# Performance work log

Hardware: AMD Instinct MI355X
Metric: run time of the kernel (lower is better)

The kernel has to match this reference:

```python
import jax, jax.numpy as jnp
import numpy as np

N_QUBITS = 4
N_LAYERS = 2
BATCH = 524288


def _apply_1q(state, U, wire, batched):
    """Apply a 2x2 gate U on `wire`. state: [B,2,2,2,2]; U: [B,2,2] if batched else [2,2]."""
    ax = wire + 1
    s = jnp.moveaxis(state, ax, 1)
    if batched:
        s = jnp.einsum('bij,bj...->bi...', U, s)
    else:
        s = jnp.einsum('ij,bj...->bi...', U, s)
    return jnp.moveaxis(s, 1, ax)


def _apply_cnot(state, control, target):
    cax, tax = control + 1, target + 1
    s0 = jnp.take(state, 0, axis=cax)
    s1 = jnp.take(state, 1, axis=cax)
    t_ax = tax - 1 if tax > cax else tax  # target axis after removing control axis
    s1 = jnp.flip(s1, axis=t_ax)
    return jnp.stack([s0, s1], axis=cax)


def _circuit(x, weight):
    B = x.shape[0]
    # Angle encoding: RY(tanh(x_i) * pi) per wire (per-sample angles)
    theta = jnp.tanh(x) * jnp.pi  # [B, 4]
    state = jnp.zeros((B,) + (2,) * N_QUBITS, jnp.complex64)
    state = state.at[(slice(None),) + (0,) * N_QUBITS].set(1.0)
    for q in range(N_QUBITS):
        h = theta[:, q] * 0.5
        c, s = jnp.cos(h), jnp.sin(h)
        Ury = jnp.stack([jnp.stack([c, -s], -1), jnp.stack([s, c], -1)], -2).astype(jnp.complex64)  # [B,2,2]
        state = _apply_1q(state, Ury, q, batched=True)
    for layer in range(N_LAYERS):
        for q in range(N_QUBITS):
            hy = weight[layer, q, 0] * 0.5
            cy, sy = jnp.cos(hy), jnp.sin(hy)
            Uy = jnp.stack([jnp.stack([cy, -sy]), jnp.stack([sy, cy])]).astype(jnp.complex64)
            state = _apply_1q(state, Uy, q, batched=False)
            hz = weight[layer, q, 1] * 0.5
            ez = jnp.exp(-1j * hz.astype(jnp.complex64))
            z0 = jnp.zeros((), jnp.complex64)
            Uz = jnp.stack([jnp.stack([ez, z0]), jnp.stack([z0, jnp.conj(ez)])])
            state = _apply_1q(state, Uz, q, batched=False)
        for q in range(N_QUBITS):
            state = _apply_cnot(state, q, (q + 1) % N_QUBITS)
    # <Z_i> = P(bit_i = 0) - P(bit_i = 1)
    probs = jnp.abs(state) ** 2  # [B,2,2,2,2] float32
    outs = []
    for q in range(N_QUBITS):
        other_axes = tuple(a for a in range(1, N_QUBITS + 1) if a != q + 1)
        marg = probs.sum(other_axes)  # [B,2]
        outs.append(marg[:, 0] - marg[:, 1])
    return jnp.stack(outs, axis=-1).astype(jnp.float32)  # [B,4]


def setup_inputs() -> dict:
    key = jax.random.key(0)
    kx, kw = jax.random.split(key)
    x = jax.random.normal(kx, (BATCH, N_QUBITS), dtype=jnp.float32)
    weight = jax.random.normal(kw, (N_LAYERS, N_QUBITS, 2), dtype=jnp.float32) * 0.1
    return {"x": x, "weight": weight}


def reference(x, weight):
    return _circuit(x, weight)
```

## Files before the change

kernel.cpp:

```cpp
#include <hip/hip_runtime.h>
#include <math.h>


#define HALF_PI_F 1.57079632679489661923f

__global__ __launch_bounds__(256) void build_C4(
    const float* __restrict__ weight,
    float4* __restrict__ C4g)
{
    __shared__ float cw[16], sw[16];
    __shared__ float Ur[16][16], Ui[16][16];
    __shared__ float A[4][16][16];

    const int tid = threadIdx.x;
    if (tid < 16) {
        float h = 0.5f * weight[tid];
        __sincosf(h, &sw[tid], &cw[tid]);
    }
    __syncthreads();

    if (tid < 16) {
        const int col = tid;
        float re[16], im[16];
        #pragma unroll
        for (int i = 0; i < 16; ++i) { re[i] = 0.f; im[i] = 0.f; }
        re[col] = 1.f;

        #pragma unroll
        for (int layer = 0; layer < 2; ++layer) {
            #pragma unroll
            for (int q = 0; q < 4; ++q) {
                float cy = cw[layer*8 + q*2 + 0];
                float sy = sw[layer*8 + q*2 + 0];
                float cz = cw[layer*8 + q*2 + 1];
                float sz = sw[layer*8 + q*2 + 1];
                int st = 8 >> q;
                #pragma unroll
                for (int i = 0; i < 16; ++i) {
                    if (i & st) continue;
                    int j = i | st;
                    float r0 = re[i], r1 = re[j], i0 = im[i], i1 = im[j];
                    float nr0 = cy*r0 - sy*r1;
                    float nr1 = sy*r0 + cy*r1;
                    float ni0 = cy*i0 - sy*i1;
                    float ni1 = sy*i0 + cy*i1;
                    re[i] = nr0*cz + ni0*sz;
                    im[i] = ni0*cz - nr0*sz;
                    re[j] = nr1*cz - ni1*sz;
                    im[j] = ni1*cz + nr1*sz;
                }
            }
            #pragma unroll
            for (int q = 0; q < 4; ++q) {
                int cb = 8 >> q;
                int tb = 8 >> ((q + 1) & 3);
                #pragma unroll
                for (int i = 0; i < 16; ++i) {
                    if ((i & cb) && !(i & tb)) {
                        int j = i | tb;
                        float tr = re[i]; re[i] = re[j]; re[j] = tr;
                        float ti = im[i]; im[i] = im[j]; im[j] = ti;
                    }
                }
            }
        }
        #pragma unroll
        for (int i = 0; i < 16; ++i) { Ur[i][col] = re[i]; Ui[i][col] = im[i]; }
    }
    __syncthreads();

    for (int e = tid; e < 1024; e += 256) {
        int q = e >> 8, j = (e >> 4) & 15, k = e & 15;
        float sum = 0.f;
        for (int i = 0; i < 16; ++i) {
            float t = Ur[i][j]*Ur[i][k] + Ui[i][j]*Ui[i][k];
            sum += (i & (8 >> q)) ? -t : t;
        }
        A[q][j][k] = sum;
    }
    __syncthreads();

    if (tid < 100) {
        const int pu[10] = {0,0,0,0,1,1,1,2,2,3};
        const int pv[10] = {0,1,2,3,1,2,3,2,3,3};
        int pi = tid / 10, qi = tid % 10;
        int u = pu[pi], v = pv[pi], r = pu[qi], sI = pv[qi];
        int a1s[2] = {u, v}, a2s[2] = {v, u};
        int b1s[2] = {r, sI}, b2s[2] = {sI, r};
        int na = (u == v) ? 1 : 2;
        int nb = (r == sI) ? 1 : 2;
        float acc[4] = {0.f, 0.f, 0.f, 0.f};
        for (int ia = 0; ia < na; ++ia)
            for (int ib = 0; ib < nb; ++ib) {
                int j = a1s[ia]*4 + b1s[ib];
                int k = a2s[ia]*4 + b2s[ib];
                #pragma unroll
                for (int q = 0; q < 4; ++q) acc[q] += A[q][j][k];
            }
        C4g[tid] = float4{acc[0], acc[1], acc[2], acc[3]};
    }
}

__global__ __launch_bounds__(256) void qmain(
    const float* __restrict__ x,
    const float4* __restrict__ C4g,
    float* __restrict__ out,
    int B)
{
    const int s0 = blockIdx.x * 256 + threadIdx.x;

    float4 xv = (s0 < B) ? reinterpret_cast<const float4*>(x)[s0]
                         : float4{0.f, 0.f, 0.f, 0.f};

    const int pu[10] = {0,0,0,0,1,1,1,2,2,3};
    const int pv[10] = {0,1,2,3,1,2,3,2,3,3};

    float P[10], Q[10];
    {
        float xs[4] = {xv.x, xv.y, xv.z, xv.w};
        float c[4], s[4];
        #pragma unroll
        for (int q = 0; q < 4; ++q) {
            float e = __expf(2.f * xs[q]);
            float uu = __builtin_amdgcn_rcpf(e + 1.f);
            float rr = 0.5f * uu;
            c[q] = __builtin_amdgcn_sinf(rr);
            s[q] = __builtin_amdgcn_cosf(rr);
        }
        float a4[4] = {c[0]*c[1], c[0]*s[1], s[0]*c[1], s[0]*s[1]};
        float b4[4] = {c[2]*c[3], c[2]*s[3], s[2]*c[3], s[2]*s[3]};
        #pragma unroll
        for (int i2 = 0; i2 < 10; ++i2) {
            P[i2] = a4[pu[i2]] * a4[pv[i2]];
            Q[i2] = b4[pu[i2]] * b4[pv[i2]];
        }
    }

    float z0 = 0.f, z1 = 0.f, z2 = 0.f, z3 = 0.f;
    #pragma unroll
    for (int pi = 0; pi < 10; ++pi) {
        float t0 = 0.f, t1 = 0.f, t2 = 0.f, t3 = 0.f;
        #pragma unroll
        for (int qi = 0; qi < 10; ++qi) {
            float4 cv = C4g[pi*10 + qi];
            float qv = Q[qi];
            t0 = fmaf(cv.x, qv, t0);
            t1 = fmaf(cv.y, qv, t1);
            t2 = fmaf(cv.z, qv, t2);
            t3 = fmaf(cv.w, qv, t3);
        }
        float pvf = P[pi];
        z0 = fmaf(pvf, t0, z0);
        z1 = fmaf(pvf, t1, z1);
        z2 = fmaf(pvf, t2, z2);
        z3 = fmaf(pvf, t3, z3);
    }

    if (s0 < B)
        reinterpret_cast<float4*>(out)[s0] = float4{z0, z1, z2, z3};
}

extern "C" void kernel_launch(void* const* d_in, const int* in_sizes, int n_in,
                              void* d_out, int out_size, void* d_ws, size_t ws_size,
                              hipStream_t stream) {
    const float* x = (const float*)d_in[0];
    const float* w = (const float*)d_in[1];
    float* out = (float*)d_out;
    float4* C4g = (float4*)d_ws;
    int B = in_sizes[0] / 4;

    build_C4<<<1, 256, 0, stream>>>(w, C4g);
    int grid = (B + 255) / 256;
    qmain<<<grid, 256, 0, stream>>>(x, C4g, out, B);
}
```

Measured before the change: 70.79 us.

## Apply fixed circuit unitary via fp16 MFMA instead of quadratic-form coefficients

The precompute kernel now writes the 16x16 fixed unitary (real and imaginary parts) in fp16 MFMA fragment layout, replacing the 100-entry quadratic-form coefficient table. The main kernel builds each sample's 16-amplitude product state in shared memory and multiplies it by the unitary with two 16x16x16 fp16 MFMAs per 16 samples. It then forms probabilities and reduces the Z expectations with cross-lane shuffles. This swaps about 400 scalar FMAs per sample for matrix-core work, at the cost of fp16 precision loss on the state and unitary, plus a block barrier and LDS traffic.

```diff
diff --git a/kernel.cpp b/kernel.cpp
--- a/kernel.cpp
+++ b/kernel.cpp
@@ -2,15 +2,22 @@
 #include <math.h>
 
 
-#define HALF_PI_F 1.57079632679489661923f
+typedef _Float16 f16x4 __attribute__((ext_vector_type(4)));
+typedef _Float16 f16x8 __attribute__((ext_vector_type(8)));
+typedef float f32x4 __attribute__((ext_vector_type(4)));
 
-__global__ __launch_bounds__(256) void build_C4(
+static __device__ inline unsigned pk16(float a, float b) {
+    unsigned short ua = __builtin_bit_cast(unsigned short, (_Float16)a);
+    unsigned short ub = __builtin_bit_cast(unsigned short, (_Float16)b);
+    return (unsigned)ua | ((unsigned)ub << 16);
+}
+
+__global__ __launch_bounds__(64) void build_U(
     const float* __restrict__ weight,
-    float4* __restrict__ C4g)
+    uint2* __restrict__ UF)
 {
     __shared__ float cw[16], sw[16];
     __shared__ float Ur[16][16], Ui[16][16];
-    __shared__ float A[4][16][16];
 
     const int tid = threadIdx.x;
     if (tid < 16) {
@@ -69,56 +76,36 @@
     }
     __syncthreads();
 
-    for (int e = tid; e < 1024; e += 256) {
-        int q = e >> 8, j = (e >> 4) & 15, k = e & 15;
-        float sum = 0.f;
-        for (int i = 0; i < 16; ++i) {
-            float t = Ur[i][j]*Ur[i][k] + Ui[i][j]*Ui[i][k];
-            sum += (i & (8 >> q)) ? -t : t;
-        }
-        A[q][j][k] = sum;
-    }
-    __syncthreads();
-
-    if (tid < 100) {
-        const int pu[10] = {0,0,0,0,1,1,1,2,2,3};
-        const int pv[10] = {0,1,2,3,1,2,3,2,3,3};
-        int pi = tid / 10, qi = tid % 10;
-        int u = pu[pi], v = pv[pi], r = pu[qi], sI = pv[qi];
-        int a1s[2] = {u, v}, a2s[2] = {v, u};
-        int b1s[2] = {r, sI}, b2s[2] = {sI, r};
-        int na = (u == v) ? 1 : 2;
-        int nb = (r == sI) ? 1 : 2;
-        float acc[4] = {0.f, 0.f, 0.f, 0.f};
-        for (int ia = 0; ia < na; ++ia)
-            for (int ib = 0; ib < nb; ++ib) {
-                int j = a1s[ia]*4 + b1s[ib];
-                int k = a2s[ia]*4 + b2s[ib];
-                #pragma unroll
-                for (int q = 0; q < 4; ++q) acc[q] += A[q][j][k];
-            }
-        C4g[tid] = float4{acc[0], acc[1], acc[2], acc[3]};
+    {
+        int m = tid & 15, k0 = (tid >> 4) << 2;
+        UF[tid]      = uint2{pk16(Ur[m][k0], Ur[m][k0+1]),
+                             pk16(Ur[m][k0+2], Ur[m][k0+3])};
+        UF[64 + tid] = uint2{pk16(Ui[m][k0], Ui[m][k0+1]),
+                             pk16(Ui[m][k0+2], Ui[m][k0+3])};
     }
 }
 
 __global__ __launch_bounds__(256) void qmain(
     const float* __restrict__ x,
-    const float4* __restrict__ C4g,
+    const uint2* __restrict__ UF,
     float* __restrict__ out,
     int B)
 {
-    const int s0 = blockIdx.x * 256 + threadIdx.x;
+    __shared__ _Float16 S[256][16];
+
+    const int tid  = threadIdx.x;
+    const int lane = tid & 63;
+    const int s0   = blockIdx.x * 256 + tid;
 
     float4 xv = (s0 < B) ? reinterpret_cast<const float4*>(x)[s0]
                          : float4{0.f, 0.f, 0.f, 0.f};
 
-    const int pu[10] = {0,0,0,0,1,1,1,2,2,3};
-    const int pv[10] = {0,1,2,3,1,2,3,2,3,3};
+    uint2 ur2 = UF[lane];
+    uint2 ui2 = UF[64 + lane];
 
-    float P[10], Q[10];
+    float c[4], s[4];
     {
         float xs[4] = {xv.x, xv.y, xv.z, xv.w};
-        float c[4], s[4];
         #pragma unroll
         for (int q = 0; q < 4; ++q) {
             float e = __expf(2.f * xs[q]);
@@ -127,37 +114,57 @@
             c[q] = __builtin_amdgcn_sinf(rr);
             s[q] = __builtin_amdgcn_cosf(rr);
         }
-        float a4[4] = {c[0]*c[1], c[0]*s[1], s[0]*c[1], s[0]*s[1]};
-        float b4[4] = {c[2]*c[3], c[2]*s[3], s[2]*c[3], s[2]*s[3]};
-        #pragma unroll
-        for (int i2 = 0; i2 < 10; ++i2) {
-            P[i2] = a4[pu[i2]] * a4[pv[i2]];
-            Q[i2] = b4[pu[i2]] * b4[pv[i2]];
-        }
     }
+    float a4[4] = {c[0]*c[1], c[0]*s[1], s[0]*c[1], s[0]*s[1]};
+    float b4[4] = {c[2]*c[3], c[2]*s[3], s[2]*c[3], s[2]*s[3]};
 
-    float z0 = 0.f, z1 = 0.f, z2 = 0.f, z3 = 0.f;
+    f16x8 lo, hi;
     #pragma unroll
-    for (int pi = 0; pi < 10; ++pi) {
-        float t0 = 0.f, t1 = 0.f, t2 = 0.f, t3 = 0.f;
-        #pragma unroll
-        for (int qi = 0; qi < 10; ++qi) {
-            float4 cv = C4g[pi*10 + qi];
-            float qv = Q[qi];
-            t0 = fmaf(cv.x, qv, t0);
-            t1 = fmaf(cv.y, qv, t1);
-            t2 = fmaf(cv.z, qv, t2);
-            t3 = fmaf(cv.w, qv, t3);
-        }
-        float pvf = P[pi];
-        z0 = fmaf(pvf, t0, z0);
-        z1 = fmaf(pvf, t1, z1);
-        z2 = fmaf(pvf, t2, z2);
-        z3 = fmaf(pvf, t3, z3);
+    for (int i = 0; i < 8; ++i)  lo[i] = (_Float16)(a4[i >> 2] * b4[i & 3]);
+    #pragma unroll
+    for (int i = 8; i < 16; ++i) hi[i - 8] = (_Float16)(a4[i >> 2] * b4[i & 3]);
+    *reinterpret_cast<f16x8*>(&S[tid][0]) = lo;
+    *reinterpret_cast<f16x8*>(&S[tid][8]) = hi;
+    __syncthreads();
+
+    f16x4 afr = __builtin_bit_cast(f16x4, ur2);
+    f16x4 afi = __builtin_bit_cast(f16x4, ui2);
+
+    const int lg = lane >> 4;
+    const int n  = lane & 15;
+    const float sg1 = (lg & 1) ? -1.f : 1.f;
+    const float sg0 = (lg & 2) ? -1.f : 1.f;
+    const int wrow = tid & 192;
+    const int wbase = blockIdx.x * 256 + wrow;
+
+    #pragma unroll
+    for (int g = 0; g < 4; ++g) {
+        f16x4 bf = *reinterpret_cast<const f16x4*>(&S[wrow + g*16 + n][lg << 2]);
+
+        f32x4 zero = {0.f, 0.f, 0.f, 0.f};
+        f32x4 dre = __builtin_amdgcn_mfma_f32_16x16x16f16(afr, bf, zero, 0, 0, 0);
+        f32x4 dim = __builtin_amdgcn_mfma_f32_16x16x16f16(afi, bf, zero, 0, 0, 0);
+
+        float m0 = dre[0]*dre[0] + dim[0]*dim[0];
+        float m1 = dre[1]*dre[1] + dim[1]*dim[1];
+        float m2 = dre[2]*dre[2] + dim[2]*dim[2];
+        float m3 = dre[3]*dre[3] + dim[3]*dim[3];
+
+        float sum = (m0 + m1) + (m2 + m3);
+        float z3 = (m0 - m1) + (m2 - m3);
+        float z2 = (m0 + m1) - (m2 + m3);
+        float z1 = sg1 * sum;
+        float z0 = sg0 * sum;
+
+        z0 += __shfl_xor(z0, 16); z0 += __shfl_xor(z0, 32);
+        z1 += __shfl_xor(z1, 16); z1 += __shfl_xor(z1, 32);
+        z2 += __shfl_xor(z2, 16); z2 += __shfl_xor(z2, 32);
+        z3 += __shfl_xor(z3, 16); z3 += __shfl_xor(z3, 32);
+
+        int samp = wbase + g*16 + n;
+        if (lg == g && samp < B)
+            reinterpret_cast<float4*>(out)[samp] = float4{z0, z1, z2, z3};
     }
-
-    if (s0 < B)
-        reinterpret_cast<float4*>(out)[s0] = float4{z0, z1, z2, z3};
 }
 
 extern "C" void kernel_launch(void* const* d_in, const int* in_sizes, int n_in,
@@ -166,10 +173,10 @@
     const float* x = (const float*)d_in[0];
     const float* w = (const float*)d_in[1];
     float* out = (float*)d_out;
-    float4* C4g = (float4*)d_ws;
+    uint2* UF = (uint2*)d_ws;
     int B = in_sizes[0] / 4;
 
-    build_C4<<<1, 256, 0, stream>>>(w, C4g);
+    build_U<<<1, 64, 0, stream>>>(w, UF);
     int grid = (B + 255) / 256;
-    qmain<<<grid, 256, 0, stream>>>(x, C4g, out, B);
+    qmain<<<grid, 256, 0, stream>>>(x, UF, out, B);
 }
```

Result: faster. 68.71 us (-2.9%).
